# Kernel tuning notes

Hardware: AMD Instinct MI355X
Metric: run time of the kernel (lower is better)

## Reference

```python
import jax, jax.numpy as jnp
import numpy as np

EMBED_DIM = 768
NUM_HEADS = 12
HEAD_DIM = EMBED_DIM // NUM_HEADS
SCALE = HEAD_DIM ** -0.5


def setup_inputs() -> dict:
    key = jax.random.key(0)
    k_x, k_qkv, k_pw, k_pb = jax.random.split(key, 4)
    B, N = 2, 4096
    x = jax.random.normal(k_x, (B, N, EMBED_DIM), dtype=jnp.float32)
    # nn.Linear weights stored as [out, in]; we keep [in, out] for x @ W
    w_qkv = jax.random.normal(k_qkv, (EMBED_DIM, 3 * EMBED_DIM), dtype=jnp.float32) * (EMBED_DIM ** -0.5)
    w_proj = jax.random.normal(k_pw, (EMBED_DIM, EMBED_DIM), dtype=jnp.float32) * (EMBED_DIM ** -0.5)
    b_proj = jax.random.normal(k_pb, (EMBED_DIM,), dtype=jnp.float32) * 0.02
    return {"x": x, "w_qkv": w_qkv, "w_proj": w_proj, "b_proj": b_proj}


def reference(x, w_qkv, w_proj, b_proj):
    B, N, D = x.shape
    H, hd = NUM_HEADS, HEAD_DIM
    qkv = x @ w_qkv                                   # [B, N, 3*D]
    qkv = qkv.reshape(B, N, 3, H, hd)                 # matches '(qkv h d)' split order
    q, k, v = (qkv[:, :, i].transpose(0, 2, 1, 3) for i in range(3))  # each [B, H, N, hd]
    attn = jnp.einsum('bhid,bhjd->bhij', q, k) * SCALE  # [B, H, N, N] fully materialized
    attn = jax.nn.softmax(attn, axis=-1)
    out = jnp.einsum('bhij,bhjd->bhid', attn, v)        # [B, H, N, hd]
    out = out.transpose(0, 2, 1, 3).reshape(B, N, D)    # 'b h n d -> b n (h d)'
    return out @ w_proj + b_proj
```

## Files before the change

### kernel.cpp

```cpp
#include <hip/hip_runtime.h>
#include <hip/hip_bf16.h>

typedef __attribute__((ext_vector_type(4))) float f32x4;
typedef __attribute__((ext_vector_type(4))) int i32x4;
typedef __attribute__((ext_vector_type(8))) short s16x8;

static constexpr int NB = 2, NH = 12, SEQ = 4096, DM = 768, HD = 64;
static constexpr int ROWS = NB * SEQ;
static constexpr float QSC = 0.125f * 1.44269504f;

#define MFMA(a, b, c) __builtin_amdgcn_mfma_f32_16x16x32_bf16((a), (b), (c), 0, 0, 0)

typedef const void __attribute__((address_space(1)))* gas_t;
typedef void __attribute__((address_space(3)))* las_t;

__device__ __forceinline__ short f2bf(float f) {
  union { float f; unsigned u; } v; v.f = f;
  unsigned r = v.u + 0x7fffu + ((v.u >> 16) & 1u);
  return (short)(r >> 16);
}

__device__ __forceinline__ float exp2v(float x) {
  float r; asm("v_exp_f32 %0, %1" : "=v"(r) : "v"(x)); return r;
}

__global__ __launch_bounds__(256) void k_cast4(const float* __restrict__ in,
                                               short* __restrict__ out, int n4) {
  int i = blockIdx.x * 256 + threadIdx.x;
  if (i < n4) {
    float4 v = reinterpret_cast<const float4*>(in)[i];
    short4 o = { f2bf(v.x), f2bf(v.y), f2bf(v.z), f2bf(v.w) };
    reinterpret_cast<short4*>(out)[i] = o;
  }
}

__global__ __launch_bounds__(256) void k_tcast2(const float* __restrict__ in,
                                                short* __restrict__ out, int r, int c) {
  __shared__ short tile[32][33];
  int tpc = c >> 5;
  int by = blockIdx.x / tpc, bx = blockIdx.x % tpc;
  int tx = threadIdx.x & 31, ty = threadIdx.x >> 5;
#pragma unroll
  for (int i = 0; i < 4; ++i)
    tile[ty + i * 8][tx] = f2bf(in[(size_t)(by * 32 + ty + i * 8) * c + bx * 32 + tx]);
  __syncthreads();
#pragma unroll
  for (int i = 0; i < 4; ++i)
    out[(size_t)(bx * 32 + ty + i * 8) * r + by * 32 + tx] = tile[tx][ty + i * 8];
}

__device__ __forceinline__ void gemm128(const short* __restrict__ A,
                                        const short* __restrict__ Bt,
                                        int K, int row0, int col0,
                                        short As[2][4096], short Bs[2][4096],
                                        f32x4 acc[4][4]) {
  int w = threadIdx.x >> 6, l = threadIdx.x & 63;
  int q = l & 15, g = l >> 4;
  int wr = w >> 1, wc = w & 1;
  int sr = w * 16 + (l >> 2);
  int sc = (l & 3) * 8;

#define STG(buf, k0)                                                           \
  {                                                                            \
    _Pragma("unroll")                                                          \
    for (int i = 0; i < 2; ++i) {                                              \
      __builtin_amdgcn_global_load_lds(                                        \
          (gas_t)(A + (size_t)(row0 + i * 64 + sr) * K + (k0) + sc),           \
          (las_t)&As[buf][i * 2048 + w * 512], 16, 0, 0);                      \
      __builtin_amdgcn_global_load_lds(                                        \
          (gas_t)(Bt + (size_t)(col0 + i * 64 + sr) * K + (k0) + sc),          \
          (las_t)&Bs[buf][i * 2048 + w * 512], 16, 0, 0);                      \
    }                                                                          \
  }

  STG(0, 0);
  __syncthreads();
  int cur = 0;
  for (int k0 = 0; k0 < K; k0 += 32) {
    if (k0 + 32 < K) STG(cur ^ 1, k0 + 32);
    s16x8 af[4], bf[4];
#pragma unroll
    for (int m = 0; m < 4; ++m)
      af[m] = *reinterpret_cast<const s16x8*>(&As[cur][(wr * 64 + m * 16 + q) * 32 + g * 8]);
#pragma unroll
    for (int n = 0; n < 4; ++n)
      bf[n] = *reinterpret_cast<const s16x8*>(&Bs[cur][(wc * 64 + n * 16 + q) * 32 + g * 8]);
#pragma unroll
    for (int m = 0; m < 4; ++m)
#pragma unroll
      for (int n = 0; n < 4; ++n)
        acc[m][n] = MFMA(af[m], bf[n], acc[m][n]);
    __syncthreads();
    cur ^= 1;
  }
#undef STG
}

__global__ __launch_bounds__(256) void k_gemm_qkv2(const short* __restrict__ xb,
                                                   const short* __restrict__ wt,
                                                   short* __restrict__ qw,
                                                   short* __restrict__ kw,
                                                   short* __restrict__ vtw) {
  __shared__ __align__(16) short As[2][4096], Bs[2][4096];
  int bid = blockIdx.x;
  int swz = (bid & 7) * 144 + (bid >> 3);
  int brow = swz / 18, bcol = swz % 18;
  int row0 = brow * 128, col0 = bcol * 128;
  f32x4 acc[4][4] = {};
  gemm128(xb, wt, DM, row0, col0, As, Bs, acc);

  int w = threadIdx.x >> 6, l = threadIdx.x & 63;
  int q = l & 15, g = l >> 4;
  int wr = w >> 1, wc = w & 1;
  int cb = col0 + wc * 64;
  int which = cb / DM, h = (cb % DM) >> 6;
  int rowb = row0 + wr * 64;
  int b = rowb >> 12;
  int bh = b * NH + h;
#pragma unroll
  for (int m = 0; m < 4; ++m) {
#pragma unroll
    for (int n = 0; n < 4; ++n) {
      int d = n * 16 + q;
      if (which == 2) {
        int nseq = (rowb & 4095) + m * 16 + g * 4;
        short4 ov = { f2bf(acc[m][n][0]), f2bf(acc[m][n][1]),
                      f2bf(acc[m][n][2]), f2bf(acc[m][n][3]) };
        *reinterpret_cast<short4*>(&vtw[((size_t)bh * HD + d) * SEQ + nseq]) = ov;
      } else {
        short* dst = (which == 0) ? qw : kw;
        float sc = (which == 0) ? QSC : 1.f;
#pragma unroll
        for (int r = 0; r < 4; ++r) {
          int nseq = (rowb & 4095) + m * 16 + g * 4 + r;
          dst[((size_t)bh * SEQ + nseq) * HD + d] = f2bf(acc[m][n][r] * sc);
        }
      }
    }
  }
}

__global__ __launch_bounds__(256) void k_gemm_proj2(const short* __restrict__ aob,
                                                    const short* __restrict__ wt,
                                                    const float* __restrict__ bias,
                                                    float* __restrict__ out) {
  __shared__ __align__(16) short As[2][4096], Bs[2][4096];
  int bid = blockIdx.x;
  int swz = (bid & 7) * 48 + (bid >> 3);
  int brow = swz / 6, bcol = swz % 6;
  int row0 = brow * 128, col0 = bcol * 128;
  f32x4 acc[4][4] = {};
  gemm128(aob, wt, DM, row0, col0, As, Bs, acc);

  int w = threadIdx.x >> 6, l = threadIdx.x & 63;
  int q = l & 15, g = l >> 4;
  int wr = w >> 1, wc = w & 1;
#pragma unroll
  for (int m = 0; m < 4; ++m)
#pragma unroll
    for (int n = 0; n < 4; ++n) {
      int col = col0 + wc * 64 + n * 16 + q;
      float bv = bias[col];
#pragma unroll
      for (int r = 0; r < 4; ++r) {
        int row = row0 + wr * 64 + m * 16 + g * 4 + r;
        out[(size_t)row * DM + col] = acc[m][n][r] + bv;
      }
    }
}

__global__ __launch_bounds__(256, 4) void k_attn12(const short* __restrict__ qw,
                                                   const short* __restrict__ kw,
                                                   const short* __restrict__ vtw,
                                                   short* __restrict__ ao) {
  __shared__ __align__(16) short lds[2][2][4096];

  int bid = blockIdx.x;
  int swz = (bid & 7) * 96 + (bid >> 3);
  int bh = swz >> 5;
  int qchunk = swz & 31;

  int w = threadIdx.x >> 6, l = threadIdx.x & 63;
  int q = l & 15, g = l >> 4;

  const short* Kg = kw + (size_t)bh * SEQ * HD;
  const short* Vg = vtw + (size_t)bh * HD * SEQ;

  int ss = (l & 7) ^ (l >> 3) ^ ((w & 1) << 2);
  int rst = w * 8 + (l >> 3);

  int qbase = qchunk * 128 + w * 32;
  s16x8 qf[2][2];
#pragma unroll
  for (int qt2 = 0; qt2 < 2; ++qt2)
#pragma unroll
    for (int kh = 0; kh < 2; ++kh)
      qf[qt2][kh] = *reinterpret_cast<const s16x8*>(
          qw + ((size_t)bh * SEQ + qbase + qt2 * 16 + q) * HD + kh * 32 + g * 8);

  s16x8 ones;
  {
    short o1 = (q == 0) ? (short)0x3F80 : (short)0;
#pragma unroll
    for (int i = 0; i < 8; ++i) ones[i] = o1;
  }

  f32x4 o[2][4] = {};
  f32x4 lsa[2] = {};

#define STAGE(buf, t)                                                              \
  {                                                                                \
    int key0 = (t) * 64;                                                           \
    _Pragma("unroll")                                                              \
    for (int i = 0; i < 2; ++i) {                                                  \
      const short* gk = Kg + (size_t)(key0 + i * 32 + rst) * HD + ss * 8;          \
      __builtin_amdgcn_global_load_lds((gas_t)gk,                                  \
          (las_t)&lds[buf][0][i * 2048 + w * 512], 16, 0, 0);                      \
      const short* gv = Vg + (size_t)(i * 32 + rst) * SEQ + key0 + ss * 8;         \
      __builtin_amdgcn_global_load_lds((gas_t)gv,                                  \
          (las_t)&lds[buf][1][i * 2048 + w * 512], 16, 0, 0);                      \
    }                                                                              \
  }

#define TBODY(CUR, NXT, tt, DO_STAGE)                                              \
  {                                                                                \
    if (DO_STAGE) STAGE(NXT, (tt) + 1);                                            \
    f32x4 s[2][2][2] = {};                             \
    __builtin_amdgcn_s_setprio(1);                                                 \
    _Pragma("unroll")                                                              \
    for (int c = 0; c < 2; ++c)                                                    \
      _Pragma("unroll")                                                            \
      for (int ab = 0; ab < 2; ++ab) {                                             \
        int R = c * 32 + ab * 4 + ((q >> 2) << 3) + (q & 3);                       \
        int sw = (R & 7) ^ (((R >> 3) & 1) << 2);                                  \
        _Pragma("unroll")                                                          \
        for (int kh = 0; kh < 2; ++kh) {                                           \
          int slot = (kh * 4 + g) ^ sw;                                            \
          s16x8 af = *reinterpret_cast<const s16x8*>(                              \
              &lds[CUR][0][R * 64 + slot * 8]);                                    \
          s[c][ab][0] = MFMA(af, qf[0][kh], s[c][ab][0]);                          \
          s[c][ab][1] = MFMA(af, qf[1][kh], s[c][ab][1]);                          \
        }                                                                          \
      }                                                                            \
    __builtin_amdgcn_s_setprio(0);                                                 \
    i32x4 pv[2][2];                                   \
    _Pragma("unroll")                                                              \
    for (int qt2 = 0; qt2 < 2; ++qt2) {                                            \
      unsigned u[16];                                                              \
      _Pragma("unroll")                                                            \
      for (int i = 0; i < 16; ++i)                                                 \
        u[i] = __float_as_uint(exp2v(s[i >> 3][(i >> 2) & 1][qt2][i & 3]));        \
      _Pragma("unroll")                                                            \
      for (int c = 0; c < 2; ++c)                                                  \
        _Pragma("unroll")                                                          \
        for (int j = 0; j < 4; ++j)                                                \
          pv[c][qt2][j] = (int)__builtin_amdgcn_perm(u[c * 8 + 2 * j + 1],         \
                                                     u[c * 8 + 2 * j],             \
                                                     0x07060302u);                 \
    }                                                                              \
    __builtin_amdgcn_s_setprio(1);                                                 \
    _Pragma("unroll")                                                              \
    for (int c = 0; c < 2; ++c) {                                                  \
      s16x8 p0 = __builtin_bit_cast(s16x8, pv[c][0]);                              \
      s16x8 p1 = __builtin_bit_cast(s16x8, pv[c][1]);                              \
      _Pragma("unroll")                                                            \
      for (int dt = 0; dt < 4; ++dt) {                                             \
        int R = dt * 16 + q;                                                       \
        int sw = (R & 7) ^ (((R >> 3) & 1) << 2);                                  \
        int slot = (c * 4 + g) ^ sw;                                               \
        s16x8 vf = *reinterpret_cast<const s16x8*>(                                \
            &lds[CUR][1][R * 64 + slot * 8]);                                      \
        o[0][dt] = MFMA(vf, p0, o[0][dt]);                                         \
        o[1][dt] = MFMA(vf, p1, o[1][dt]);                                         \
      }                                                                            \
      lsa[0] = MFMA(ones, p0, lsa[0]);                                             \
      lsa[1] = MFMA(ones, p1, lsa[1]);                                             \
    }                                                                              \
    __builtin_amdgcn_s_setprio(0);                                                 \
    __syncthreads();                                                               \
  }

  STAGE(0, 0);
  __syncthreads();

  for (int t = 0; t < SEQ / 64 - 2; t += 2) {
    TBODY(0, 1, t, true);
    TBODY(1, 0, t + 1, true);
  }
  TBODY(0, 1, SEQ / 64 - 2, true);
  TBODY(1, 0, SEQ / 64 - 1, false);
#undef TBODY
#undef STAGE

  int b = bh / NH, h = bh % NH;
  float ls0 = __shfl(lsa[0][0], q);
  float ls1 = __shfl(lsa[1][0], q);
  float inv[2] = { 1.f / ls0, 1.f / ls1 };
#pragma unroll
  for (int qt2 = 0; qt2 < 2; ++qt2) {
    size_t row = (size_t)b * SEQ + qbase + qt2 * 16 + q;
    short* op = ao + row * DM + h * HD;
#pragma unroll
    for (int dt = 0; dt < 4; ++dt) {
      short4 ov = { f2bf(o[qt2][dt][0] * inv[qt2]), f2bf(o[qt2][dt][1] * inv[qt2]),
                    f2bf(o[qt2][dt][2] * inv[qt2]), f2bf(o[qt2][dt][3] * inv[qt2]) };
      *reinterpret_cast<short4*>(op + dt * 16 + g * 4) = ov;
    }
  }
}

extern "C" void kernel_launch(void* const* d_in, const int* in_sizes, int n_in,
                              void* d_out, int out_size, void* d_ws, size_t ws_size,
                              hipStream_t stream) {
  const float* x      = (const float*)d_in[0];
  const float* w_qkv  = (const float*)d_in[1];
  const float* w_proj = (const float*)d_in[2];
  const float* b_proj = (const float*)d_in[3];
  float* out = (float*)d_out;

  char* p = (char*)d_ws;
  auto take = [&](size_t bytes) { char* r = p; p += (bytes + 255) & ~(size_t)255; return r; };
  short* xb     = (short*)take((size_t)ROWS * DM * 2);
  short* wtqkv  = (short*)take((size_t)3 * DM * DM * 2);
  short* wtproj = (short*)take((size_t)DM * DM * 2);
  short* qw     = (short*)take((size_t)NB * NH * SEQ * HD * 2);
  short* kw     = (short*)take((size_t)NB * NH * SEQ * HD * 2);
  short* vtw    = (short*)take((size_t)NB * NH * HD * SEQ * 2);
  short* ao     = (short*)take((size_t)ROWS * DM * 2);

  int n4 = ROWS * DM / 4;
  k_cast4<<<(n4 + 255) / 256, 256, 0, stream>>>(x, xb, n4);
  k_tcast2<<<(DM / 32) * (3 * DM / 32), 256, 0, stream>>>(w_qkv, wtqkv, DM, 3 * DM);
  k_tcast2<<<(DM / 32) * (DM / 32), 256, 0, stream>>>(w_proj, wtproj, DM, DM);
  k_gemm_qkv2<<<64 * 18, 256, 0, stream>>>(xb, wtqkv, qw, kw, vtw);
  k_attn12<<<NB * NH * (SEQ / 128), 256, 0, stream>>>(qw, kw, vtw, ao);
  k_gemm_proj2<<<64 * 6, 256, 0, stream>>>(ao, wtproj, b_proj, out);
}
```

Measured before the change: 179.4 us.

## Double query rows per attention block to reuse K/V tiles

Each attention workgroup now processes 256 query rows (64 per wave) instead of 128, so every K/V tile staged into LDS and every LDS fragment read feeds twice as many MFMAs. This halves global K/V traffic and LDS reads per unit of work. The cost is roughly double the accumulator and score registers, hence launch bounds drop to 2 blocks per CU, and the grid shrinks to 384 blocks, which lowers occupancy and the latency hiding it gives.

```diff
diff --git a/kernel.cpp b/kernel.cpp
--- a/kernel.cpp
+++ b/kernel.cpp
@@ -169,16 +169,16 @@
     }
 }
 
-__global__ __launch_bounds__(256, 4) void k_attn12(const short* __restrict__ qw,
+__global__ __launch_bounds__(256, 2) void k_attn13(const short* __restrict__ qw,
                                                    const short* __restrict__ kw,
                                                    const short* __restrict__ vtw,
                                                    short* __restrict__ ao) {
   __shared__ __align__(16) short lds[2][2][4096];
 
   int bid = blockIdx.x;
-  int swz = (bid & 7) * 96 + (bid >> 3);
-  int bh = swz >> 5;
-  int qchunk = swz & 31;
+  int swz = (bid & 7) * 48 + (bid >> 3);
+  int bh = swz >> 4;
+  int qchunk = swz & 15;
 
   int w = threadIdx.x >> 6, l = threadIdx.x & 63;
   int q = l & 15, g = l >> 4;
@@ -189,14 +189,14 @@
   int ss = (l & 7) ^ (l >> 3) ^ ((w & 1) << 2);
   int rst = w * 8 + (l >> 3);
 
-  int qbase = qchunk * 128 + w * 32;
-  s16x8 qf[2][2];
-#pragma unroll
-  for (int qt2 = 0; qt2 < 2; ++qt2)
+  int qbase = qchunk * 256 + w * 64;
+  s16x8 qf[4][2];
+#pragma unroll
+  for (int qt = 0; qt < 4; ++qt)
 #pragma unroll
     for (int kh = 0; kh < 2; ++kh)
-      qf[qt2][kh] = *reinterpret_cast<const s16x8*>(
-          qw + ((size_t)bh * SEQ + qbase + qt2 * 16 + q) * HD + kh * 32 + g * 8);
+      qf[qt][kh] = *reinterpret_cast<const s16x8*>(
+          qw + ((size_t)bh * SEQ + qbase + qt * 16 + q) * HD + kh * 32 + g * 8);
 
   s16x8 ones;
   {
@@ -205,8 +205,8 @@
     for (int i = 0; i < 8; ++i) ones[i] = o1;
   }
 
-  f32x4 o[2][4] = {};
-  f32x4 lsa[2] = {};
+  f32x4 o[4][4] = {};
+  f32x4 lsa[4] = {};
 
 #define STAGE(buf, t)                                                              \
   {                                                                                \
@@ -225,7 +225,7 @@
 #define TBODY(CUR, NXT, tt, DO_STAGE)                                              \
   {                                                                                \
     if (DO_STAGE) STAGE(NXT, (tt) + 1);                                            \
-    f32x4 s[2][2][2] = {};                             \
+    f32x4 s[2][2][4] = {};                              \
     __builtin_amdgcn_s_setprio(1);                                                 \
     _Pragma("unroll")                                                              \
     for (int c = 0; c < 2; ++c)                                                    \
@@ -238,31 +238,30 @@
           int slot = (kh * 4 + g) ^ sw;                                            \
           s16x8 af = *reinterpret_cast<const s16x8*>(                              \
               &lds[CUR][0][R * 64 + slot * 8]);                                    \
-          s[c][ab][0] = MFMA(af, qf[0][kh], s[c][ab][0]);                          \
-          s[c][ab][1] = MFMA(af, qf[1][kh], s[c][ab][1]);                          \
+          _Pragma("unroll")                                                        \
+          for (int qt = 0; qt < 4; ++qt)                                           \
+            s[c][ab][qt] = MFMA(af, qf[qt][kh], s[c][ab][qt]);                     \
         }                                                                          \
       }                                                                            \
     __builtin_amdgcn_s_setprio(0);                                                 \
-    i32x4 pv[2][2];                                   \
+    i32x4 pv[2][4];                                    \
     _Pragma("unroll")                                                              \
-    for (int qt2 = 0; qt2 < 2; ++qt2) {                                            \
+    for (int qt = 0; qt < 4; ++qt) {                                               \
       unsigned u[16];                                                              \
       _Pragma("unroll")                                                            \
       for (int i = 0; i < 16; ++i)                                                 \
-        u[i] = __float_as_uint(exp2v(s[i >> 3][(i >> 2) & 1][qt2][i & 3]));        \
+        u[i] = __float_as_uint(exp2v(s[i >> 3][(i >> 2) & 1][qt][i & 3]));         \
       _Pragma("unroll")                                                            \
       for (int c = 0; c < 2; ++c)                                                  \
         _Pragma("unroll")                                                          \
         for (int j = 0; j < 4; ++j)                                                \
-          pv[c][qt2][j] = (int)__builtin_amdgcn_perm(u[c * 8 + 2 * j + 1],         \
-                                                     u[c * 8 + 2 * j],             \
-                                                     0x07060302u);                 \
+          pv[c][qt][j] = (int)__builtin_amdgcn_perm(u[c * 8 + 2 * j + 1],          \
+                                                    u[c * 8 + 2 * j],              \
+                                                    0x07060302u);                  \
     }                                                                              \
     __builtin_amdgcn_s_setprio(1);                                                 \
     _Pragma("unroll")                                                              \
     for (int c = 0; c < 2; ++c) {                                                  \
-      s16x8 p0 = __builtin_bit_cast(s16x8, pv[c][0]);                              \
-      s16x8 p1 = __builtin_bit_cast(s16x8, pv[c][1]);                              \
       _Pragma("unroll")                                                            \
       for (int dt = 0; dt < 4; ++dt) {                                             \
         int R = dt * 16 + q;                                                       \
@@ -270,11 +269,13 @@
         int slot = (c * 4 + g) ^ sw;                                               \
         s16x8 vf = *reinterpret_cast<const s16x8*>(                                \
             &lds[CUR][1][R * 64 + slot * 8]);                                      \
-        o[0][dt] = MFMA(vf, p0, o[0][dt]);                                         \
-        o[1][dt] = MFMA(vf, p1, o[1][dt]);                                         \
+        _Pragma("unroll")                                                          \
+        for (int qt = 0; qt < 4; ++qt)                                             \
+          o[qt][dt] = MFMA(vf, __builtin_bit_cast(s16x8, pv[c][qt]), o[qt][dt]);   \
       }                                                                            \
-      lsa[0] = MFMA(ones, p0, lsa[0]);                                             \
-      lsa[1] = MFMA(ones, p1, lsa[1]);                                             \
+      _Pragma("unroll")                                                            \
+      for (int qt = 0; qt < 4; ++qt)                                               \
+        lsa[qt] = MFMA(ones, __builtin_bit_cast(s16x8, pv[c][qt]), lsa[qt]);       \
     }                                                                              \
     __builtin_amdgcn_s_setprio(0);                                                 \
     __syncthreads();                                                               \
@@ -293,17 +294,16 @@
 #undef STAGE
 
   int b = bh / NH, h = bh % NH;
-  float ls0 = __shfl(lsa[0][0], q);
-  float ls1 = __shfl(lsa[1][0], q);
-  float inv[2] = { 1.f / ls0, 1.f / ls1 };
-#pragma unroll
-  for (int qt2 = 0; qt2 < 2; ++qt2) {
-    size_t row = (size_t)b * SEQ + qbase + qt2 * 16 + q;
+#pragma unroll
+  for (int qt = 0; qt < 4; ++qt) {
+    float ls = __shfl(lsa[qt][0], q);
+    float inv = 1.f / ls;
+    size_t row = (size_t)b * SEQ + qbase + qt * 16 + q;
     short* op = ao + row * DM + h * HD;
 #pragma unroll
     for (int dt = 0; dt < 4; ++dt) {
-      short4 ov = { f2bf(o[qt2][dt][0] * inv[qt2]), f2bf(o[qt2][dt][1] * inv[qt2]),
-                    f2bf(o[qt2][dt][2] * inv[qt2]), f2bf(o[qt2][dt][3] * inv[qt2]) };
+      short4 ov = { f2bf(o[qt][dt][0] * inv), f2bf(o[qt][dt][1] * inv),
+                    f2bf(o[qt][dt][2] * inv), f2bf(o[qt][dt][3] * inv) };
       *reinterpret_cast<short4*>(op + dt * 16 + g * 4) = ov;
     }
   }
@@ -333,6 +333,6 @@
   k_tcast2<<<(DM / 32) * (3 * DM / 32), 256, 0, stream>>>(w_qkv, wtqkv, DM, 3 * DM);
   k_tcast2<<<(DM / 32) * (DM / 32), 256, 0, stream>>>(w_proj, wtproj, DM, DM);
   k_gemm_qkv2<<<64 * 18, 256, 0, stream>>>(xb, wtqkv, qw, kw, vtw);
-  k_attn12<<<NB * NH * (SEQ / 128), 256, 0, stream>>>(qw, kw, vtw, ao);
+  k_attn13<<<NB * NH * (SEQ / 256), 256, 0, stream>>>(qw, kw, vtw, ao);
   k_gemm_proj2<<<64 * 6, 256, 0, stream>>>(ao, wtproj, b_proj, out);
 }
```

Result: slower. 192.4 us (+7.3%).

## Merge prep casts into one launch and transpose MFMA operands for vector stores

Applied to the files above, without the earlier changes.

Folds the three input cast and transpose kernels into a single k_prep launch, which removes two kernel launches and their tail gaps. The MFMA operands in the shared GEMM are swapped so each lane's accumulator holds four consecutive columns, not four consecutive rows. Q/K and the projection output can then be written as packed short4 and float4 stores, and bias is loaded as a vector. The V-transpose output now goes out as scalar strided stores, which may cost more on that third of the QKV epilogue.

```diff
diff --git a/kernel.cpp b/kernel.cpp
--- a/kernel.cpp
+++ b/kernel.cpp
@@ -24,21 +24,15 @@
   float r; asm("v_exp_f32 %0, %1" : "=v"(r) : "v"(x)); return r;
 }
 
-__global__ __launch_bounds__(256) void k_cast4(const float* __restrict__ in,
-                                               short* __restrict__ out, int n4) {
-  int i = blockIdx.x * 256 + threadIdx.x;
-  if (i < n4) {
-    float4 v = reinterpret_cast<const float4*>(in)[i];
-    short4 o = { f2bf(v.x), f2bf(v.y), f2bf(v.z), f2bf(v.w) };
-    reinterpret_cast<short4*>(out)[i] = o;
-  }
-}
-
-__global__ __launch_bounds__(256) void k_tcast2(const float* __restrict__ in,
-                                                short* __restrict__ out, int r, int c) {
-  __shared__ short tile[32][33];
+static constexpr int NC4 = ROWS * DM / 4 / 256;
+static constexpr int NT1 = (DM / 32) * (3 * DM / 32);
+static constexpr int NT2 = (DM / 32) * (DM / 32);
+
+__device__ __forceinline__ void tcast_body(const float* __restrict__ in,
+                                           short* __restrict__ out, int r, int c,
+                                           int bid, short tile[32][33]) {
   int tpc = c >> 5;
-  int by = blockIdx.x / tpc, bx = blockIdx.x % tpc;
+  int by = bid / tpc, bx = bid % tpc;
   int tx = threadIdx.x & 31, ty = threadIdx.x >> 5;
 #pragma unroll
   for (int i = 0; i < 4; ++i)
@@ -47,6 +41,26 @@
 #pragma unroll
   for (int i = 0; i < 4; ++i)
     out[(size_t)(bx * 32 + ty + i * 8) * r + by * 32 + tx] = tile[tx][ty + i * 8];
+}
+
+__global__ __launch_bounds__(256) void k_prep(const float* __restrict__ x,
+                                              short* __restrict__ xb,
+                                              const float* __restrict__ wqkv,
+                                              short* __restrict__ wtqkv,
+                                              const float* __restrict__ wproj,
+                                              short* __restrict__ wtproj) {
+  __shared__ short tile[32][33];
+  int bid = blockIdx.x;
+  if (bid < NC4) {
+    int i = bid * 256 + threadIdx.x;
+    float4 v = reinterpret_cast<const float4*>(x)[i];
+    short4 o = { f2bf(v.x), f2bf(v.y), f2bf(v.z), f2bf(v.w) };
+    reinterpret_cast<short4*>(xb)[i] = o;
+  } else if (bid < NC4 + NT1) {
+    tcast_body(wqkv, wtqkv, DM, 3 * DM, bid - NC4, tile);
+  } else {
+    tcast_body(wproj, wtproj, DM, DM, bid - NC4 - NT1, tile);
+  }
 }
 
 __device__ __forceinline__ void gemm128(const short* __restrict__ A,
@@ -89,7 +103,7 @@
     for (int m = 0; m < 4; ++m)
 #pragma unroll
       for (int n = 0; n < 4; ++n)
-        acc[m][n] = MFMA(af[m], bf[n], acc[m][n]);
+        acc[m][n] = MFMA(bf[n], af[m], acc[m][n]);
     __syncthreads();
     cur ^= 1;
   }
@@ -119,22 +133,20 @@
   int bh = b * NH + h;
 #pragma unroll
   for (int m = 0; m < 4; ++m) {
+    int nseq = (rowb & 4095) + m * 16 + q;
 #pragma unroll
     for (int n = 0; n < 4; ++n) {
-      int d = n * 16 + q;
+      int d = n * 16 + g * 4;
       if (which == 2) {
-        int nseq = (rowb & 4095) + m * 16 + g * 4;
-        short4 ov = { f2bf(acc[m][n][0]), f2bf(acc[m][n][1]),
-                      f2bf(acc[m][n][2]), f2bf(acc[m][n][3]) };
-        *reinterpret_cast<short4*>(&vtw[((size_t)bh * HD + d) * SEQ + nseq]) = ov;
+#pragma unroll
+        for (int r = 0; r < 4; ++r)
+          vtw[((size_t)bh * HD + d + r) * SEQ + nseq] = f2bf(acc[m][n][r]);
       } else {
         short* dst = (which == 0) ? qw : kw;
         float sc = (which == 0) ? QSC : 1.f;
-#pragma unroll
-        for (int r = 0; r < 4; ++r) {
-          int nseq = (rowb & 4095) + m * 16 + g * 4 + r;
-          dst[((size_t)bh * SEQ + nseq) * HD + d] = f2bf(acc[m][n][r] * sc);
-        }
+        short4 ov = { f2bf(acc[m][n][0] * sc), f2bf(acc[m][n][1] * sc),
+                      f2bf(acc[m][n][2] * sc), f2bf(acc[m][n][3] * sc) };
+        *reinterpret_cast<short4*>(&dst[((size_t)bh * SEQ + nseq) * HD + d]) = ov;
       }
     }
   }
@@ -156,17 +168,16 @@
   int q = l & 15, g = l >> 4;
   int wr = w >> 1, wc = w & 1;
 #pragma unroll
-  for (int m = 0; m < 4; ++m)
+  for (int m = 0; m < 4; ++m) {
+    int row = row0 + wr * 64 + m * 16 + q;
 #pragma unroll
     for (int n = 0; n < 4; ++n) {
-      int col = col0 + wc * 64 + n * 16 + q;
-      float bv = bias[col];
-#pragma unroll
-      for (int r = 0; r < 4; ++r) {
-        int row = row0 + wr * 64 + m * 16 + g * 4 + r;
-        out[(size_t)row * DM + col] = acc[m][n][r] + bv;
-      }
+      int col = col0 + wc * 64 + n * 16 + g * 4;
+      f32x4 bv = *reinterpret_cast<const f32x4*>(&bias[col]);
+      f32x4 ov = acc[m][n] + bv;
+      *reinterpret_cast<f32x4*>(&out[(size_t)row * DM + col]) = ov;
     }
+  }
 }
 
 __global__ __launch_bounds__(256, 4) void k_attn12(const short* __restrict__ qw,
@@ -328,10 +339,7 @@
   short* vtw    = (short*)take((size_t)NB * NH * HD * SEQ * 2);
   short* ao     = (short*)take((size_t)ROWS * DM * 2);
 
-  int n4 = ROWS * DM / 4;
-  k_cast4<<<(n4 + 255) / 256, 256, 0, stream>>>(x, xb, n4);
-  k_tcast2<<<(DM / 32) * (3 * DM / 32), 256, 0, stream>>>(w_qkv, wtqkv, DM, 3 * DM);
-  k_tcast2<<<(DM / 32) * (DM / 32), 256, 0, stream>>>(w_proj, wtproj, DM, DM);
+  k_prep<<<NC4 + NT1 + NT2, 256, 0, stream>>>(x, xb, w_qkv, wtqkv, w_proj, wtproj);
   k_gemm_qkv2<<<64 * 18, 256, 0, stream>>>(xb, wtqkv, qw, kw, vtw);
   k_attn12<<<NB * NH * (SEQ / 128), 256, 0, stream>>>(qw, kw, vtw, ao);
   k_gemm_proj2<<<64 * 6, 256, 0, stream>>>(ao, wtproj, b_proj, out);
```

After: 177.0 us. Within noise of the previous version (-1.3%).
